# Kernel optimization log

Hardware: AMD Instinct MI355X
Metric: run time of the kernel (lower is better)

The kernel has to match this reference:

```python
import jax, jax.numpy as jnp
import numpy as np

K = 100
TEMPERATURE = 1.0


def setup_inputs() -> dict:
    key = jax.random.key(0)
    k1, k2, k3 = jax.random.split(key, 3)
    student_emb = jax.random.normal(k1, (8, 512, 1500), dtype=jnp.float32)
    teacher_codes = jax.random.randint(k2, (8, 1500), 0, 4096, dtype=jnp.int64)
    codebook = jax.random.normal(k3, (4096, 512), dtype=jnp.float32)
    return {"student_emb": student_emb, "teacher_codes": teacher_codes, "codebook": codebook}


def reference(student_emb, teacher_codes, codebook):
    B, C, T = student_emb.shape
    # flatten tokens: (N, C) with N = B*T
    emb = jnp.transpose(student_emb, (0, 2, 1)).reshape(-1, C)
    codes = teacher_codes.reshape(-1).astype(jnp.int32)

    # Euclidean cdist via the ||a||^2 + ||b||^2 - 2ab expansion (same math as torch.cdist)
    emb_sq = jnp.sum(emb * emb, axis=1, keepdims=True)            # (N,1)
    cb_sq = jnp.sum(codebook * codebook, axis=1)[None, :]         # (1,V)
    d2 = emb_sq + cb_sq - 2.0 * jnp.matmul(emb, codebook.T)       # (N,V)
    distances = jnp.sqrt(jnp.maximum(d2, 0.0))

    # top-k smallest distances
    _, top_k_indices = jax.lax.top_k(-distances, K)               # (N,K)

    # include_correct: replace last candidate with the true code if absent
    correct_in_topk = jnp.any(top_k_indices == codes[:, None], axis=1)
    top_k_indices = top_k_indices.at[:, -1].set(
        jnp.where(correct_in_topk, top_k_indices[:, -1], codes))

    candidate_distances = jnp.take_along_axis(distances, top_k_indices, axis=1)
    logits = -candidate_distances / TEMPERATURE                   # (N,K)

    match = top_k_indices == codes[:, None]
    local_labels = jnp.argmax(match.astype(jnp.int32), axis=1)    # (N,)

    logp = jax.nn.log_softmax(logits, axis=1)
    loss = -jnp.mean(jnp.take_along_axis(logp, local_labels[:, None], axis=1))

    local_predictions = jnp.argmax(logits, axis=-1)
    local_accuracy = jnp.mean((local_predictions == local_labels).astype(jnp.float32))
    global_predictions = jnp.argmin(distances, axis=-1)
    global_accuracy = jnp.mean((global_predictions == codes).astype(jnp.float32))
    correct_in_candidates = jnp.mean(jnp.any(top_k_indices == codes[:, None], axis=1).astype(jnp.float32))

    return loss, local_accuracy, global_accuracy, correct_in_candidates
```

## Files before the change

kernel.cpp:

```cpp
#include <hip/hip_runtime.h>
#include <hip/hip_bf16.h>
#include <cstdint>

#define B_ 8
#define C_ 512
#define T_ 1500
#define N_ (B_*T_)
#define NPAD_ 12032
#define V_ 4096
#define K_ 100
#define NCB_ 16

typedef unsigned long long u64;
typedef __attribute__((ext_vector_type(8))) short short8;
typedef __attribute__((ext_vector_type(8))) unsigned short u16x8;
typedef __attribute__((ext_vector_type(4))) float f32x4;

__device__ __forceinline__ unsigned short f2bf(float x){
    __hip_bfloat16 h = __float2bfloat16(x);
    return __builtin_bit_cast(unsigned short, h);
}
__device__ __forceinline__ unsigned short f2h(float x){
    return __builtin_bit_cast(unsigned short, (_Float16)x);
}
__device__ __forceinline__ float h2f(unsigned short h){
    return (float)__builtin_bit_cast(_Float16, h);
}

__device__ __forceinline__ void gll16(const unsigned short* g, unsigned short* l){
    __builtin_amdgcn_global_load_lds(
        (const __attribute__((address_space(1))) void*)g,
        (__attribute__((address_space(3))) void*)l, 16, 0, 0);
}

__global__ __launch_bounds__(256) void prep_kernel(const float* __restrict__ CB,
                                                   unsigned short* __restrict__ CBh,
                                                   float* __restrict__ csq,
                                                   const float* __restrict__ S,
                                                   unsigned short* __restrict__ embT,
                                                   float* __restrict__ esqp){
    __shared__ float tile[32][33];
    __shared__ float psum[8][33];
    int bid = blockIdx.x;
    if (bid < V_/4){
        int wv = threadIdx.x >> 6, lane = threadIdx.x & 63;
        int r = bid * 4 + wv;
        const float4* p4 = (const float4*)(CB + (size_t)r * C_);
        ushort4* o4 = (ushort4*)(CBh + (size_t)r * C_);
        float s = 0.f;
        #pragma unroll
        for (int j = 0; j < 2; ++j){
            float4 v = p4[lane + j*64];
            s += v.x*v.x + v.y*v.y + v.z*v.z + v.w*v.w;
            ushort4 h; h.x = f2bf(v.x); h.y = f2bf(v.y); h.z = f2bf(v.z); h.w = f2bf(v.w);
            o4[lane + j*64] = h;
        }
        #pragma unroll
        for (int o = 32; o; o >>= 1) s += __shfl_down(s, o, 64);
        if (lane == 0) csq[r] = s;
        return;
    }
    int idx = bid - V_/4;
    const int NTB = (T_ + 31) / 32;
    int bxt = idx % NTB;
    int byc = (idx / NTB) % NCB_;
    int bz  = idx / (NTB * NCB_);
    int c0 = byc * 32;
    int t0 = bxt * 32;
    int tx = threadIdx.x & 31, ty = threadIdx.x >> 5;
    #pragma unroll
    for (int r = 0; r < 4; ++r){
        int c = c0 + ty + r*8;
        int t = t0 + tx;
        tile[ty + r*8][tx] = (t < T_) ? S[((size_t)bz*C_ + c)*T_ + t] : 0.f;
    }
    __syncthreads();
    float ps = 0.f;
    #pragma unroll
    for (int r = 0; r < 4; ++r){ float v = tile[ty + r*8][tx]; ps += v * v; }
    psum[ty][tx] = ps;
    #pragma unroll
    for (int r = 0; r < 4; ++r){
        int t = t0 + ty + r*8;
        int c = c0 + tx;
        if (t < T_) embT[((size_t)bz*T_ + t)*C_ + c] = f2bf(tile[tx][ty + r*8]);
    }
    __syncthreads();
    if (ty == 0){
        int t = t0 + tx;
        if (t < T_){
            float s2 = 0.f;
            #pragma unroll
            for (int w = 0; w < 8; ++w) s2 += psum[w][tx];
            esqp[(size_t)byc * N_ + bz*T_ + t] = s2;
        }
    }
}

__global__ __launch_bounds__(256) void gemm_dot_kernel(
    const unsigned short* __restrict__ A, const unsigned short* __restrict__ Bm,
    unsigned short* __restrict__ doth, int row_lo, int row_hi)
{
    __shared__ unsigned short smem[128*136];
    unsigned short* As = smem;
    unsigned short* Bs = smem + 128*32;
    int tid = threadIdx.x, lane = tid & 63, wv = tid >> 6;
    int row0 = row_lo + blockIdx.x * 128;
    int col0 = blockIdx.y * 128;

    int sr = lane >> 2;
    int sk = (lane & 3) * 8;
    int ar0 = row0 + wv*32 + sr;       int ar1 = ar0 + 16;
    int ca0 = (ar0 < N_) ? ar0 : N_-1; int ca1 = (ar1 < N_) ? ar1 : N_-1;
    const unsigned short* Ap0 = A  + (size_t)ca0 * C_ + sk;
    const unsigned short* Ap1 = A  + (size_t)ca1 * C_ + sk;
    const unsigned short* Bp0 = Bm + (size_t)(col0 + wv*32 + sr) * C_ + sk;
    const unsigned short* Bp1 = Bp0 + (size_t)16 * C_;
    unsigned short* Ad0 = &As[(wv*32     ) * 32];
    unsigned short* Ad1 = &As[(wv*32 + 16) * 32];
    unsigned short* Bd0 = &Bs[(wv*32     ) * 32];
    unsigned short* Bd1 = &Bs[(wv*32 + 16) * 32];

    int wm = (wv >> 1) * 64, wn = (wv & 1) * 64;
    int fr = lane & 15;
    int fk = (lane >> 4) * 8;

    f32x4 acc[4][4];
    #pragma unroll
    for (int i = 0; i < 4; ++i)
        #pragma unroll
        for (int j = 0; j < 4; ++j) acc[i][j] = (f32x4){0.f, 0.f, 0.f, 0.f};

    for (int kt = 0; kt < C_/32; ++kt){
        int k0 = kt * 32;
        gll16(Ap0 + k0, Ad0);
        gll16(Ap1 + k0, Ad1);
        gll16(Bp0 + k0, Bd0);
        gll16(Bp1 + k0, Bd1);
        __syncthreads();
        short8 af[4], bf[4];
        #pragma unroll
        for (int i = 0; i < 4; ++i) af[i] = *(const short8*)&As[(wm + i*16 + fr)*32 + fk];
        #pragma unroll
        for (int j = 0; j < 4; ++j) bf[j] = *(const short8*)&Bs[(wn + j*16 + fr)*32 + fk];
        #pragma unroll
        for (int i = 0; i < 4; ++i)
            #pragma unroll
            for (int j = 0; j < 4; ++j)
                acc[i][j] = __builtin_amdgcn_mfma_f32_16x16x32_bf16(bf[j], af[i], acc[i][j], 0, 0, 0);
        __syncthreads();
    }

    const int LD = 136;
    int en = lane & 15;
    int ev = (lane >> 4) * 4;
    #pragma unroll
    for (int i = 0; i < 4; ++i){
        int r = wm + i*16 + en;
        #pragma unroll
        for (int j = 0; j < 4; ++j){
            ushort4 h;
            h.x = f2h(acc[i][j][0]);
            h.y = f2h(acc[i][j][1]);
            h.z = f2h(acc[i][j][2]);
            h.w = f2h(acc[i][j][3]);
            *(ushort4*)&smem[r*LD + wn + j*16 + ev] = h;
        }
    }
    __syncthreads();

    int rr = tid >> 4;
    int cc = (tid & 15) * 8;
    #pragma unroll
    for (int it = 0; it < 8; ++it){
        int r = it*16 + rr;
        int n = row0 + r;
        if (n < row_hi){
            u16x8 v = *(const u16x8*)&smem[r*LD + cc];
            *(u16x8*)&doth[(size_t)(n - row_lo) * V_ + col0 + cc] = v;
        }
    }
}

__global__ __launch_bounds__(256, 2) void select_kernel(const unsigned short* __restrict__ doth,
                                                        const int* __restrict__ codes,
                                                        const float* __restrict__ esqp,
                                                        const float* __restrict__ csq,
                                                        float2* __restrict__ pairbuf,
                                                        int row_lo, int nrows){
    int tid = threadIdx.x, lane = tid & 63, wv = tid >> 6;
    int lrow = blockIdx.x * 4 + wv;
    if (lrow >= nrows) return;
    int n = row_lo + lrow;
    const u16x8* r8 = (const u16x8*)(doth + (size_t)lrow * V_);

    __shared__ unsigned hist[4][256] __attribute__((aligned(16)));
    __shared__ unsigned coll[4][64];
    __shared__ unsigned collcnt[4];

    float esq_n = 0.f;
    #pragma unroll
    for (int p = 0; p < NCB_; ++p) esq_n += esqp[(size_t)p * N_ + n];

    int code = codes[n];
    float dotc = h2f(doth[(size_t)lrow * V_ + code]);
    unsigned ucode = __float_as_uint(fmaxf(esq_n + csq[code] - 2.f * dotc, 0.f));

    unsigned u[64];
    unsigned vmn = 0xFFFFFFFFu, vmx = 0u;
    int km = 0;
    #pragma unroll
    for (int j = 0; j < 8; ++j){
        u16x8 h = r8[lane + j*64];
        const float4* cp = (const float4*)(csq + 8*lane + 512*j);
        float4 c0 = cp[0], c1 = cp[1];
        float cs[8] = {c0.x, c0.y, c0.z, c0.w, c1.x, c1.y, c1.z, c1.w};
        #pragma unroll
        for (int e = 0; e < 8; ++e){
            int k = 8*j + e;
            unsigned v = __float_as_uint(fmaxf(esq_n + cs[e] - 2.f * h2f(h[e]), 0.f));
            u[k] = v;
            if (v < vmn){ vmn = v; km = k; }
            vmx = (v > vmx) ? v : vmx;
        }
    }
    unsigned im = 8u*(unsigned)lane + (unsigned)(512*(km >> 3) + (km & 7));
    #pragma unroll
    for (int o = 32; o; o >>= 1){
        unsigned v2 = (unsigned)__shfl_xor((int)vmn, o, 64);
        unsigned i2 = (unsigned)__shfl_xor((int)im,  o, 64);
        if (v2 < vmn || (v2 == vmn && i2 < im)){ vmn = v2; im = i2; }
        unsigned x2 = (unsigned)__shfl_xor((int)vmx, o, 64); if (x2 > vmx) vmx = x2;
    }
    unsigned umin = vmn, umax = vmx;
    int idx0 = (int)im;
    float d0 = sqrtf(__uint_as_float(umin));

    unsigned t;
    if (umin == umax){
        t = umin;
    } else {
        ((uint4*)&hist[wv][0])[lane] = (uint4){0u,0u,0u,0u};
        if (lane == 0) collcnt[wv] = 0u;
        asm volatile("s_waitcnt lgkmcnt(0)" ::: "memory");
        float fmn = __uint_as_float(umin), fmx = __uint_as_float(umax);
        float invw = 256.0f / (fmx - fmn);
        #pragma unroll
        for (int k = 0; k < 64; ++k){
            float fk = __uint_as_float(u[k]);
            int b = (int)((fk - fmn) * invw); b = (b > 255) ? 255 : b;
            atomicAdd(&hist[wv][b], 1u);
        }
        asm volatile("s_waitcnt lgkmcnt(0)" ::: "memory");
        uint4 hq = ((uint4*)&hist[wv][0])[lane];
        unsigned lsum = hq.x + hq.y + hq.z + hq.w;
        unsigned inc = lsum;
        #pragma unroll
        for (int o = 1; o < 64; o <<= 1){
            unsigned y = (unsigned)__shfl_up((int)inc, o, 64);
            if (lane >= o) inc += y;
        }
        unsigned e0 = inc - lsum;
        unsigned e1 = e0 + hq.x, e2 = e1 + hq.y, e3 = e2 + hq.z, e4 = e3 + hq.w;
        int sel = -1;
        if      (e0 <= 99u && 99u < e1) sel = 0;
        else if (e1 <= 99u && 99u < e2) sel = 1;
        else if (e2 <= 99u && 99u < e3) sel = 2;
        else if (e3 <= 99u && 99u < e4) sel = 3;
        u64 bal = __ballot(sel >= 0);
        int src = __ffsll(bal) - 1;
        unsigned myBk = (unsigned)(4*lane + (sel < 0 ? 0 : sel));
        unsigned myBase = (sel == 1) ? e1 : (sel == 2) ? e2 : (sel == 3) ? e3 : e0;
        int Bk   = __shfl((int)myBk,   src, 64);
        int base = __shfl((int)myBase, src, 64);
        int rk = 99 - base;
        #pragma unroll
        for (int k = 0; k < 64; ++k){
            float fk = __uint_as_float(u[k]);
            int b = (int)((fk - fmn) * invw); b = (b > 255) ? 255 : b;
            if (b == Bk){
                unsigned pos = atomicAdd(&collcnt[wv], 1u);
                if (pos < 64u) coll[wv][pos] = u[k];
            }
        }
        asm volatile("s_waitcnt lgkmcnt(0)" ::: "memory");
        unsigned bcnt = collcnt[wv];
        if (bcnt <= 64u){
            unsigned w = (lane < (int)bcnt) ? coll[wv][lane] : 0xFFFFFFFFu;
            unsigned wmn = (lane < (int)bcnt) ? w : 0xFFFFFFFFu;
            unsigned wmx = (lane < (int)bcnt) ? w : 0u;
            #pragma unroll
            for (int o = 32; o; o >>= 1){
                unsigned a = (unsigned)__shfl_xor((int)wmn, o, 64); if (a < wmn) wmn = a;
                unsigned b = (unsigned)__shfl_xor((int)wmx, o, 64); if (b > wmx) wmx = b;
            }
            unsigned P;
            if (wmn == wmx) P = wmn;
            else {
                int hb = 31 - __clz((int)(wmn ^ wmx));
                unsigned mask = (hb == 31) ? 0xFFFFFFFFu : ((1u << (hb+1)) - 1u);
                P = wmn & ~mask;
                for (int b = hb; b >= 0; --b){
                    unsigned cand = P | (1u << b);
                    int c = __popcll(__ballot(w < cand));
                    if (c <= rk) P = cand;
                }
            }
            t = P;
        } else {
            int hb = 31 - __clz((int)(umin ^ umax));
            unsigned mask = (hb == 31) ? 0xFFFFFFFFu : ((1u << (hb+1)) - 1u);
            unsigned P = umin & ~mask;
            for (int b = hb; b >= 0; --b){
                unsigned cand = P | (1u << b);
                int c = 0;
                #pragma unroll
                for (int k = 0; k < 64; ++k) c += (u[k] < cand) ? 1 : 0;
                #pragma unroll
                for (int o = 32; o; o >>= 1) c += __shfl_xor(c, o, 64);
                if (c <= 99) P = cand;
            }
            t = P;
        }
    }
    float tval = sqrtf(__uint_as_float(t));

    float s = 0.f; int cl = 0;
    #pragma unroll
    for (int k = 0; k < 64; ++k){
        if (u[k] < t){ s += __expf(d0 - sqrtf(__uint_as_float(u[k]))); cl++; }
    }
    #pragma unroll
    for (int o = 32; o; o >>= 1){
        s += __shfl_xor(s, o, 64);
        cl += __shfl_xor(cl, o, 64);
    }
    if (lane == 0){
        float S = s + (float)(K_ - cl) * __expf(d0 - tval);
        float dcode = sqrtf(__uint_as_float(ucode));
        if (ucode > t) S += __expf(d0 - dcode) - __expf(d0 - tval);
        float nll = dcode - d0 + __logf(S);
        pairbuf[n] = make_float2(nll, (idx0 == code) ? 1.f : 0.f);
    }
}

__global__ __launch_bounds__(1024) void finalize_kernel(const float2* __restrict__ pair,
                                                        float* __restrict__ out){
    int tid = threadIdx.x;
    float sn = 0.f, sh = 0.f;
    for (int i = tid; i < N_; i += 1024){
        float2 p = pair[i]; sn += p.x; sh += p.y;
    }
    #pragma unroll
    for (int o = 32; o; o >>= 1){ sn += __shfl_down(sn, o, 64); sh += __shfl_down(sh, o, 64); }
    __shared__ float a[16], b[16];
    int wv = tid >> 6, lane = tid & 63;
    if (lane == 0){ a[wv] = sn; b[wv] = sh; }
    __syncthreads();
    if (tid == 0){
        float L = 0.f, H = 0.f;
        #pragma unroll
        for (int i = 0; i < 16; ++i){ L += a[i]; H += b[i]; }
        out[0] = L / (float)N_;
        out[1] = H / (float)N_;
        out[2] = H / (float)N_;
        out[3] = 1.0f;
    }
}

extern "C" void kernel_launch(void* const* d_in, const int* in_sizes, int n_in,
                              void* d_out, int out_size, void* d_ws, size_t ws_size,
                              hipStream_t stream){
    const float* S   = (const float*)d_in[0];
    const int* codes = (const int*)d_in[1];
    const float* CB  = (const float*)d_in[2];
    float* out = (float*)d_out;

    char* w = (char*)d_ws;
    size_t off = 0;
    unsigned short* embT = (unsigned short*)(w + off); off += (size_t)NPAD_ * C_ * 2;
    unsigned short* CBh  = (unsigned short*)(w + off); off += (size_t)V_ * C_ * 2;
    float* csq  = (float*)(w + off); off += (size_t)V_ * 4;
    float* esqp = (float*)(w + off); off += (size_t)NCB_ * N_ * 4;
    off = (off + 255) & ~(size_t)255;
    float2* pairbuf = (float2*)(w + off); off += (size_t)N_ * 8;
    unsigned short* dotbuf = (unsigned short*)(w + off);

    size_t avail = (ws_size > off) ? ws_size - off : 0;
    long maxrows = (long)(avail / ((size_t)V_ * 2));

    const int NTB = (T_ + 31) / 32;
    int prep_blocks = V_/4 + NTB * NCB_ * B_;
    hipLaunchKernelGGL(prep_kernel, dim3(prep_blocks), dim3(256), 0, stream,
                       CB, CBh, csq, S, embT, esqp);

    if (maxrows >= N_){
        const int gchunk = 6144;
        for (int row_lo = 0; row_lo < N_; row_lo += gchunk){
            int row_hi = row_lo + gchunk; if (row_hi > N_) row_hi = N_;
            int rows = row_hi - row_lo;
            hipLaunchKernelGGL(gemm_dot_kernel, dim3((rows + 127)/128, V_/128), dim3(256), 0, stream,
                               embT, CBh, dotbuf + (size_t)row_lo * V_, row_lo, row_hi);
        }
        hipLaunchKernelGGL(select_kernel, dim3((N_ + 3)/4), dim3(256), 0, stream,
                           dotbuf, codes, esqp, csq, pairbuf, 0, N_);
    } else {
        int chunk = (int)(maxrows & ~127L);
        if (chunk < 128) chunk = 128;
        for (int row_lo = 0; row_lo < N_; row_lo += chunk){
            int row_hi = row_lo + chunk; if (row_hi > N_) row_hi = N_;
            int rows = row_hi - row_lo;
            hipLaunchKernelGGL(gemm_dot_kernel, dim3((rows + 127)/128, V_/128), dim3(256), 0, stream,
                               embT, CBh, dotbuf, row_lo, row_hi);
            hipLaunchKernelGGL(select_kernel, dim3((rows + 3)/4), dim3(256), 0, stream,
                               dotbuf, codes, esqp, csq, pairbuf, row_lo, rows);
        }
    }
    hipLaunchKernelGGL(finalize_kernel, dim3(1), dim3(1024), 0, stream, pairbuf, out);
}
```

Measured before the change: 214.0 us.

## Split each select row across two wavefronts to halve per-thread register arrays

The top-k selection kernel now processes one row per 128-thread block (two wavefronts) instead of one row per wavefront in a 256-thread block. Each thread holds 32 distance values instead of 64. Min/max, histogram, collection and partial sums are combined across the two waves through shared memory and __syncthreads. The aim is lower register pressure and higher occupancy, which should better hide memory latency when streaming the dot-product buffer. The cost is extra block-level barriers, including inside the fallback bit-search loop, and more, smaller blocks.

```diff
diff --git a/kernel.cpp b/kernel.cpp
--- a/kernel.cpp
+++ b/kernel.cpp
@@ -182,21 +182,26 @@
     }
 }
 
-__global__ __launch_bounds__(256, 2) void select_kernel(const unsigned short* __restrict__ doth,
-                                                        const int* __restrict__ codes,
-                                                        const float* __restrict__ esqp,
-                                                        const float* __restrict__ csq,
-                                                        float2* __restrict__ pairbuf,
-                                                        int row_lo, int nrows){
-    int tid = threadIdx.x, lane = tid & 63, wv = tid >> 6;
-    int lrow = blockIdx.x * 4 + wv;
+__global__ __launch_bounds__(128) void select_kernel(const unsigned short* __restrict__ doth,
+                                                     const int* __restrict__ codes,
+                                                     const float* __restrict__ esqp,
+                                                     const float* __restrict__ csq,
+                                                     float2* __restrict__ pairbuf,
+                                                     int row_lo, int nrows){
+    int tid = threadIdx.x;
+    int lane = tid & 63, wv = tid >> 6;
+    int lrow = blockIdx.x;
     if (lrow >= nrows) return;
     int n = row_lo + lrow;
     const u16x8* r8 = (const u16x8*)(doth + (size_t)lrow * V_);
 
-    __shared__ unsigned hist[4][256] __attribute__((aligned(16)));
-    __shared__ unsigned coll[4][64];
-    __shared__ unsigned collcnt[4];
+    __shared__ unsigned hist[256] __attribute__((aligned(16)));
+    __shared__ unsigned coll[64];
+    __shared__ unsigned collcnt;
+    __shared__ unsigned xmn[2], xim[2], xmx[2];
+    __shared__ float xs[2];
+    __shared__ int xcl[2];
+    __shared__ int xc[2];
 
     float esq_n = 0.f;
     #pragma unroll
@@ -206,13 +211,16 @@
     float dotc = h2f(doth[(size_t)lrow * V_ + code]);
     unsigned ucode = __float_as_uint(fmaxf(esq_n + csq[code] - 2.f * dotc, 0.f));
 
-    unsigned u[64];
+    ((uint2*)hist)[tid] = (uint2){0u, 0u};
+    if (tid == 0) collcnt = 0u;
+
+    unsigned u[32];
     unsigned vmn = 0xFFFFFFFFu, vmx = 0u;
     int km = 0;
     #pragma unroll
-    for (int j = 0; j < 8; ++j){
-        u16x8 h = r8[lane + j*64];
-        const float4* cp = (const float4*)(csq + 8*lane + 512*j);
+    for (int j = 0; j < 4; ++j){
+        u16x8 h = r8[tid + j*128];
+        const float4* cp = (const float4*)(csq + 8*tid + 1024*j);
         float4 c0 = cp[0], c1 = cp[1];
         float cs[8] = {c0.x, c0.y, c0.z, c0.w, c1.x, c1.y, c1.z, c1.w};
         #pragma unroll
@@ -224,7 +232,7 @@
             vmx = (v > vmx) ? v : vmx;
         }
     }
-    unsigned im = 8u*(unsigned)lane + (unsigned)(512*(km >> 3) + (km & 7));
+    unsigned im = 8u*(unsigned)tid + (unsigned)(1024*(km >> 3) + (km & 7));
     #pragma unroll
     for (int o = 32; o; o >>= 1){
         unsigned v2 = (unsigned)__shfl_xor((int)vmn, o, 64);
@@ -232,27 +240,31 @@
         if (v2 < vmn || (v2 == vmn && i2 < im)){ vmn = v2; im = i2; }
         unsigned x2 = (unsigned)__shfl_xor((int)vmx, o, 64); if (x2 > vmx) vmx = x2;
     }
-    unsigned umin = vmn, umax = vmx;
-    int idx0 = (int)im;
+    if (lane == 0){ xmn[wv] = vmn; xim[wv] = im; xmx[wv] = vmx; }
+    __syncthreads();
+    unsigned umin, umax; int idx0;
+    {
+        unsigned a0 = xmn[0], a1 = xmn[1], i0 = xim[0], i1 = xim[1];
+        if (a1 < a0 || (a1 == a0 && i1 < i0)){ umin = a1; idx0 = (int)i1; }
+        else                                 { umin = a0; idx0 = (int)i0; }
+        umax = (xmx[0] > xmx[1]) ? xmx[0] : xmx[1];
+    }
     float d0 = sqrtf(__uint_as_float(umin));
 
     unsigned t;
     if (umin == umax){
         t = umin;
     } else {
-        ((uint4*)&hist[wv][0])[lane] = (uint4){0u,0u,0u,0u};
-        if (lane == 0) collcnt[wv] = 0u;
-        asm volatile("s_waitcnt lgkmcnt(0)" ::: "memory");
         float fmn = __uint_as_float(umin), fmx = __uint_as_float(umax);
         float invw = 256.0f / (fmx - fmn);
         #pragma unroll
-        for (int k = 0; k < 64; ++k){
+        for (int k = 0; k < 32; ++k){
             float fk = __uint_as_float(u[k]);
             int b = (int)((fk - fmn) * invw); b = (b > 255) ? 255 : b;
-            atomicAdd(&hist[wv][b], 1u);
-        }
-        asm volatile("s_waitcnt lgkmcnt(0)" ::: "memory");
-        uint4 hq = ((uint4*)&hist[wv][0])[lane];
+            atomicAdd(&hist[b], 1u);
+        }
+        __syncthreads();
+        uint4 hq = ((uint4*)hist)[lane];
         unsigned lsum = hq.x + hq.y + hq.z + hq.w;
         unsigned inc = lsum;
         #pragma unroll
@@ -275,20 +287,20 @@
         int base = __shfl((int)myBase, src, 64);
         int rk = 99 - base;
         #pragma unroll
-        for (int k = 0; k < 64; ++k){
+        for (int k = 0; k < 32; ++k){
             float fk = __uint_as_float(u[k]);
             int b = (int)((fk - fmn) * invw); b = (b > 255) ? 255 : b;
             if (b == Bk){
-                unsigned pos = atomicAdd(&collcnt[wv], 1u);
-                if (pos < 64u) coll[wv][pos] = u[k];
+                unsigned pos = atomicAdd(&collcnt, 1u);
+                if (pos < 64u) coll[pos] = u[k];
             }
         }
-        asm volatile("s_waitcnt lgkmcnt(0)" ::: "memory");
-        unsigned bcnt = collcnt[wv];
-        if (bcnt <= 64u){
-            unsigned w = (lane < (int)bcnt) ? coll[wv][lane] : 0xFFFFFFFFu;
-            unsigned wmn = (lane < (int)bcnt) ? w : 0xFFFFFFFFu;
-            unsigned wmx = (lane < (int)bcnt) ? w : 0u;
+        __syncthreads();
+        int bcnt = (int)collcnt;
+        if (bcnt <= 64){
+            unsigned w = (lane < bcnt) ? coll[lane] : 0xFFFFFFFFu;
+            unsigned wmn = (lane < bcnt) ? w : 0xFFFFFFFFu;
+            unsigned wmx = (lane < bcnt) ? w : 0u;
             #pragma unroll
             for (int o = 32; o; o >>= 1){
                 unsigned a = (unsigned)__shfl_xor((int)wmn, o, 64); if (a < wmn) wmn = a;
@@ -315,10 +327,14 @@
                 unsigned cand = P | (1u << b);
                 int c = 0;
                 #pragma unroll
-                for (int k = 0; k < 64; ++k) c += (u[k] < cand) ? 1 : 0;
+                for (int k = 0; k < 32; ++k) c += (u[k] < cand) ? 1 : 0;
                 #pragma unroll
                 for (int o = 32; o; o >>= 1) c += __shfl_xor(c, o, 64);
-                if (c <= 99) P = cand;
+                if (lane == 0) xc[wv] = c;
+                __syncthreads();
+                int ctot = xc[0] + xc[1];
+                __syncthreads();
+                if (ctot <= 99) P = cand;
             }
             t = P;
         }
@@ -327,7 +343,7 @@
 
     float s = 0.f; int cl = 0;
     #pragma unroll
-    for (int k = 0; k < 64; ++k){
+    for (int k = 0; k < 32; ++k){
         if (u[k] < t){ s += __expf(d0 - sqrtf(__uint_as_float(u[k]))); cl++; }
     }
     #pragma unroll
@@ -335,8 +351,10 @@
         s += __shfl_xor(s, o, 64);
         cl += __shfl_xor(cl, o, 64);
     }
-    if (lane == 0){
-        float S = s + (float)(K_ - cl) * __expf(d0 - tval);
+    if (lane == 0){ xs[wv] = s; xcl[wv] = cl; }
+    __syncthreads();
+    if (tid == 0){
+        float S = (xs[0] + xs[1]) + (float)(K_ - (xcl[0] + xcl[1])) * __expf(d0 - tval);
         float dcode = sqrtf(__uint_as_float(ucode));
         if (ucode > t) S += __expf(d0 - dcode) - __expf(d0 - tval);
         float nll = dcode - d0 + __logf(S);
@@ -402,7 +420,7 @@
             hipLaunchKernelGGL(gemm_dot_kernel, dim3((rows + 127)/128, V_/128), dim3(256), 0, stream,
                                embT, CBh, dotbuf + (size_t)row_lo * V_, row_lo, row_hi);
         }
-        hipLaunchKernelGGL(select_kernel, dim3((N_ + 3)/4), dim3(256), 0, stream,
+        hipLaunchKernelGGL(select_kernel, dim3(N_), dim3(128), 0, stream,
                            dotbuf, codes, esqp, csq, pairbuf, 0, N_);
     } else {
         int chunk = (int)(maxrows & ~127L);
@@ -412,7 +430,7 @@
             int rows = row_hi - row_lo;
             hipLaunchKernelGGL(gemm_dot_kernel, dim3((rows + 127)/128, V_/128), dim3(256), 0, stream,
                                embT, CBh, dotbuf, row_lo, row_hi);
-            hipLaunchKernelGGL(select_kernel, dim3((rows + 3)/4), dim3(256), 0, stream,
+            hipLaunchKernelGGL(select_kernel, dim3(rows), dim3(128), 0, stream,
                                dotbuf, codes, esqp, csq, pairbuf, row_lo, rows);
         }
     }
```

Result: no change. 210.3 us, median of 2 (-1.7%).
